# Kernel optimization log

Measured on AMD Instinct MI355X. Metric: run time of the kernel, lower is better.

Reference implementation:

```python
import jax, jax.numpy as jnp
import numpy as np

NEG = -1.0e30  # finite stand-in for -inf (exp(NEG-x)==0 exactly in fp32, grad-safe)
PRUNE = 5


def setup_inputs() -> dict:
    key = jax.random.key(0)
    k1, k2, k3, k4 = jax.random.split(key, 4)
    B, T, U, V = 8, 192, 193, 512
    logits = jax.random.normal(k1, (B, T, U, V), dtype=jnp.float32)
    log_probs = jax.nn.log_softmax(logits, axis=-1)  # [B,T,U,V]
    targets = jax.random.randint(k2, (B, U - 1), 1, V, dtype=jnp.int32)
    # lengths must satisfy |t_len-u_len| <= PRUNE for the terminal cell to be in-band
    target_lengths = jax.random.randint(k3, (B,), 150, U, dtype=jnp.int32)
    off = jax.random.randint(k4, (B,), -3, 4, dtype=jnp.int32)
    logit_lengths = jnp.clip(target_lengths + off, 1, T).astype(jnp.int32)
    return {"log_probs": log_probs, "targets": targets,
            "logit_lengths": logit_lengths, "target_lengths": target_lengths}


def _rnnt_loss(log_probs, targets, logit_lengths, target_lengths, prune_range=PRUNE):
    B, T, U, V = log_probs.shape
    Ut = targets.shape[1]  # U - 1
    dt = log_probs.dtype

    blank = log_probs[..., 0]  # [B,T,U] p_blank at (t,u)
    # emit[b,t,j] = log_probs[b,t,j,targets[b,j]]
    emit = jnp.take_along_axis(log_probs[:, :, :Ut, :], targets[:, None, :, None], axis=3)[..., 0]  # [B,T,Ut]
    # emit candidate requires t < T: pad a NEG row at t==T
    emit = jnp.concatenate([emit, jnp.full((B, 1, Ut), NEG, dt)], axis=1)  # [B,T+1,Ut]
    # g[b,t,u] = gain entering cell (t,u) from (t,u-1); g[:,:,0] unused
    g_all = jnp.concatenate([jnp.full((B, T + 1, 1), NEG, dt), emit], axis=2)  # [B,T+1,U]
    # blank_pad[:,t,:] = blank[:,t-1,:] (row t pulls blank from frame t-1); t==0 has no blank move
    blank_pad = jnp.concatenate([jnp.full((B, 1, U), NEG, dt), blank], axis=1)  # [B,T+1,U]

    u_idx = jnp.arange(U)

    def band_mask(t):
        # cells the original actually computes on row t
        return ((u_idx[None, :] >= t - prune_range)
                & (u_idx[None, :] <= t + prune_range)
                & (u_idx[None, :] <= target_lengths[:, None]))

    def combine(x, y):
        # linear recurrence r[u] = logaddexp(r[u-1] + g[u], base[u]) as an associative op
        g1, r1 = x
        g2, r2 = y
        return (g1 + g2, jnp.logaddexp(r1 + g2, r2))

    def row_from_base(base, g, t):
        base = jnp.where(band_mask(t), base, NEG)  # out-of-band cells never feed the row
        _, r = jax.lax.associative_scan(combine, (g, base), axis=1)
        return jnp.where(band_mask(t), r, NEG)

    # row 0: alpha[0,0]=0, within-row emit chain
    init_base = jnp.full((B, U), NEG, dt).at[:, 0].set(0.0)
    row0 = row_from_base(init_base, g_all[:, 0], 0)

    def step(prev, xs):
        blank_row, g_row, t = xs
        row = row_from_base(prev + blank_row, g_row, t)  # blank move from row t-1, then emit chain
        return row, row

    ts = jnp.arange(1, T + 1)
    _, rows = jax.lax.scan(step, row0,
                           (blank_pad[:, 1:].transpose(1, 0, 2),
                            g_all[:, 1:].transpose(1, 0, 2), ts))
    rows = jnp.concatenate([row0[None], rows], axis=0)  # [T+1,B,U]

    final = rows[logit_lengths, jnp.arange(B), target_lengths]  # alpha[t_len, u_len]
    return jnp.mean(-final)  # reduction='mean'


def reference(log_probs, targets, logit_lengths, target_lengths):
    return _rnnt_loss(log_probs, targets, logit_lengths, target_lengths)
```

## Files before the change

### kernel.cpp

```cpp
#include <hip/hip_runtime.h>


#define NEGV -1.0e30f
#define LOG2E 1.4426950408889634f
#define LN2   0.6931471805599453f

constexpr int Bc = 8, Tc = 192, Uc = 193, Vc = 512;
constexpr int Utc = Uc - 1;
constexpr int NCH = 16;
constexpr int CL  = 12;

#if __has_builtin(__builtin_amdgcn_exp2f)
#define EXP2(x) __builtin_amdgcn_exp2f(x)
#else
#define EXP2(x) __expf((x) * LN2)
#endif
#if __has_builtin(__builtin_amdgcn_logf)
#define LOG2(x) __builtin_amdgcn_logf(x)
#else
#define LOG2(x) (__logf(x) * LOG2E)
#endif

template <int CTRL>
__device__ __forceinline__ float dppf(float old, float x) {
    return __int_as_float(__builtin_amdgcn_update_dpp(
        __float_as_int(old), __float_as_int(x), CTRL, 0xF, 0xF, false));
}

__device__ __forceinline__ float lae2(float a, float b) {
    float m = fmaxf(a, b);
    float d = fminf(a, b) - m;
    return m + LOG2(1.0f + EXP2(d));
}

__device__ __forceinline__ float prefix_sum16(float g) {
    g += dppf<0x111>(0.0f, g);
    g += dppf<0x112>(0.0f, g);
    g += dppf<0x114>(0.0f, g);
    g += dppf<0x118>(0.0f, g);
    return g;
}

__device__ __forceinline__ float prefix_lae16(float s) {
    s = lae2(dppf<0x111>(NEGV, s), s);
    s = lae2(dppf<0x112>(NEGV, s), s);
    s = lae2(dppf<0x114>(NEGV, s), s);
    s = lae2(dppf<0x118>(NEGV, s), s);
    return s;
}

__device__ __forceinline__ float row_update(float alpha, float2 cur, int t,
                                            int tlen, int ls) {
    float base = dppf<0x101>(NEGV, alpha) + cur.x;
    float res;
    if (t == Tc) {
        res = base;
    } else {
        float G = prefix_sum16(cur.y);
        res = prefix_lae16(base - G) + G;
    }
    int u = t - 5 + ls;
    bool valid = (ls <= 10) && (u >= 0) && (u <= tlen);
    return valid ? res : NEGV;
}

__global__ void __launch_bounds__(192) rnnt_chunk_kernel(
        const float* __restrict__ lp, const int* __restrict__ targets,
        const int* __restrict__ logit_len, const int* __restrict__ target_len,
        float* __restrict__ ws) {
    __shared__ float2 rowbuf[CL * 16];

    const int b = blockIdx.x >> 4;
    const int c = blockIdx.x & 15;
    const int llen = logit_len[b];
    const int tlen = target_len[b];
    const int t0 = 1 + c * CL;

    {
        const int idx = threadIdx.x;
        const int r = idx >> 4, d = idx & 15;
        const int t = t0 + r;
        if (t <= llen) {
            const int u = t - 5 + d;
            float bl = NEGV;
            float g = 0.0f;
            if (d <= 10 && u >= 0 && u <= Uc - 1)
                bl = lp[(((size_t)b * Tc + (t - 1)) * Uc + u) * Vc] * LOG2E;
            if (d <= 10 && u >= 1 && u <= Uc - 1 && t <= Tc - 1)
                g = lp[(((size_t)b * Tc + t) * Uc + (u - 1)) * Vc
                       + targets[b * Utc + (u - 1)]] * LOG2E;
            rowbuf[idx] = make_float2(bl, g);
        }
    }
    __syncthreads();

    const int j  = threadIdx.x >> 4;
    const int ls = threadIdx.x & 15;
    if (j >= 11) return;

    float alpha = (ls == j) ? 0.0f : NEGV;
    #pragma unroll
    for (int r = 0; r < CL; ++r) {
        const int t = t0 + r;
        if (t > llen) break;
        alpha = row_update(alpha, rowbuf[r * 16 + ls], t, tlen, ls);
    }
    ws[(((size_t)(b * NCH + c) * 11 + j) << 4) + ls] = alpha;
}

__global__ void __launch_bounds__(64) rnnt_final_kernel(
        const float* __restrict__ lp, const int* __restrict__ targets,
        const int* __restrict__ logit_len, const int* __restrict__ target_len,
        const float* __restrict__ ws, float* __restrict__ out) {
    const int b = blockIdx.x;
    const int llen = logit_len[b];
    const int tlen = target_len[b];
    const int lane = threadIdx.x;
    const int ls = lane & 15;

    float g = 0.0f;
    {
        const int u = ls - 5;
        if (ls <= 10 && u >= 1)
            g = lp[((size_t)b * Tc * Uc + (u - 1)) * Vc
                   + targets[b * Utc + (u - 1)]] * LOG2E;
    }
    float v;
    {
        float G = prefix_sum16(g);
        float base = (ls == 5) ? 0.0f : NEGV;
        float res = prefix_lae16(base - G) + G;
        const int u = ls - 5;
        const bool valid = (ls <= 10) && (u >= 0) && (u <= tlen);
        v = valid ? res : NEGV;
    }

    for (int c = 0; c < NCH; ++c) {
        const size_t off = ((size_t)(b * NCH + c) * 11) << 4;
        float cand[11];
        #pragma unroll
        for (int jj = 0; jj < 11; ++jj) {
            float m = ws[off + ((size_t)jj << 4) + ls];
            float vj = __int_as_float(
                __builtin_amdgcn_readlane(__float_as_int(v), jj));
            cand[jj] = m + vj;
        }
        float a0 = lae2(cand[0], cand[1]);
        float a1 = lae2(cand[2], cand[3]);
        float a2 = lae2(cand[4], cand[5]);
        float a3 = lae2(cand[6], cand[7]);
        float a4 = lae2(cand[8], cand[9]);
        float b0 = lae2(a0, a1);
        float b1 = lae2(a2, a3);
        float b2 = lae2(a4, cand[10]);
        v = lae2(lae2(b0, b1), b2);
    }

    if (lane == tlen - llen + 5)
        atomicAdd(out, v * (-LN2 / (float)Bc));
}

extern "C" void kernel_launch(void* const* d_in, const int* in_sizes, int n_in,
                              void* d_out, int out_size, void* d_ws, size_t ws_size,
                              hipStream_t stream) {
    const float* lp    = (const float*)d_in[0];
    const int* targets = (const int*)d_in[1];
    const int* llen    = (const int*)d_in[2];
    const int* tlen    = (const int*)d_in[3];
    float* out = (float*)d_out;

    hipMemsetAsync(out, 0, sizeof(float) * out_size, stream);
    rnnt_chunk_kernel<<<Bc * NCH, 192, 0, stream>>>(
        lp, targets, llen, tlen, (float*)d_ws);
    rnnt_final_kernel<<<Bc, 64, 0, stream>>>(
        lp, targets, llen, tlen, (const float*)d_ws, out);
}
```

Baseline: 648.5 us.

## Fuse chunk and final kernels into one per-batch block with shared-memory transfer matrices

Replaces the two-kernel scheme (128 chunk blocks writing transfer matrices to a global workspace, then 8 final blocks combining them) with a single kernel that uses one 896-thread block per batch element. Each block gathers all band values for its sequence into shared memory. It then computes 5 chunk transfer matrices of 39 rows each in parallel and combines them in-block. This removes a kernel launch and the global workspace round-trip. In exchange it uses only 8 blocks on the GPU, each thread issues several serial gather loads, and the per-chunk serial recurrence is more than three times longer.

```diff
diff --git a/kernel.cpp b/kernel.cpp
--- a/kernel.cpp
+++ b/kernel.cpp
@@ -7,8 +7,10 @@
 
 constexpr int Bc = 8, Tc = 192, Uc = 193, Vc = 512;
 constexpr int Utc = Uc - 1;
-constexpr int NCH = 16;
-constexpr int CL  = 12;
+constexpr int ROWS = Tc + 1;
+constexpr int NCH = 5;
+constexpr int CL  = 39;
+constexpr int NTHR = 896;
 
 #if __has_builtin(__builtin_amdgcn_exp2f)
 #define EXP2(x) __builtin_amdgcn_exp2f(x)
@@ -64,83 +66,62 @@
     return valid ? res : NEGV;
 }
 
-__global__ void __launch_bounds__(192) rnnt_chunk_kernel(
+__global__ void __launch_bounds__(NTHR) rnnt_fused_kernel(
         const float* __restrict__ lp, const int* __restrict__ targets,
         const int* __restrict__ logit_len, const int* __restrict__ target_len,
-        float* __restrict__ ws) {
-    __shared__ float2 rowbuf[CL * 16];
+        float* __restrict__ out) {
+    __shared__ float2 rowbuf[ROWS * 16];
+    __shared__ float  mat[NCH * 11 * 16];
 
-    const int b = blockIdx.x >> 4;
-    const int c = blockIdx.x & 15;
+    const int b = blockIdx.x;
     const int llen = logit_len[b];
     const int tlen = target_len[b];
-    const int t0 = 1 + c * CL;
+    const int nrows = llen + 1;
 
-    {
-        const int idx = threadIdx.x;
-        const int r = idx >> 4, d = idx & 15;
-        const int t = t0 + r;
-        if (t <= llen) {
-            const int u = t - 5 + d;
-            float bl = NEGV;
-            float g = 0.0f;
-            if (d <= 10 && u >= 0 && u <= Uc - 1)
-                bl = lp[(((size_t)b * Tc + (t - 1)) * Uc + u) * Vc] * LOG2E;
-            if (d <= 10 && u >= 1 && u <= Uc - 1 && t <= Tc - 1)
-                g = lp[(((size_t)b * Tc + t) * Uc + (u - 1)) * Vc
-                       + targets[b * Utc + (u - 1)]] * LOG2E;
-            rowbuf[idx] = make_float2(bl, g);
-        }
+    for (int idx = threadIdx.x; idx < nrows * 16; idx += NTHR) {
+        int t = idx >> 4, d = idx & 15;
+        int u = t - 5 + d;
+        float bl = NEGV;
+        float g = 0.0f;
+        if (d <= 10 && u >= 0 && u <= Uc - 1 && t >= 1)
+            bl = lp[(((size_t)b * Tc + (t - 1)) * Uc + u) * Vc] * LOG2E;
+        if (d <= 10 && u >= 1 && u <= Uc - 1 && t <= Tc - 1)
+            g = lp[(((size_t)b * Tc + t) * Uc + (u - 1)) * Vc
+                   + targets[b * Utc + (u - 1)]] * LOG2E;
+        rowbuf[idx] = make_float2(bl, g);
     }
     __syncthreads();
 
-    const int j  = threadIdx.x >> 4;
+    const int e  = threadIdx.x >> 4;
     const int ls = threadIdx.x & 15;
-    if (j >= 11) return;
+    if (e < NCH * 11) {
+        const int c = e / 11, j = e - c * 11;
+        const int t0 = 1 + c * CL;
+        const int tend = min(t0 + CL - 1, llen);
+        float alpha = (ls == j) ? 0.0f : NEGV;
+        for (int t = t0; t <= tend; ++t)
+            alpha = row_update(alpha, rowbuf[t * 16 + ls], t, tlen, ls);
+        mat[e * 16 + ls] = alpha;
+    }
+    __syncthreads();
 
-    float alpha = (ls == j) ? 0.0f : NEGV;
-    #pragma unroll
-    for (int r = 0; r < CL; ++r) {
-        const int t = t0 + r;
-        if (t > llen) break;
-        alpha = row_update(alpha, rowbuf[r * 16 + ls], t, tlen, ls);
-    }
-    ws[(((size_t)(b * NCH + c) * 11 + j) << 4) + ls] = alpha;
-}
+    if (threadIdx.x >= 64) return;
 
-__global__ void __launch_bounds__(64) rnnt_final_kernel(
-        const float* __restrict__ lp, const int* __restrict__ targets,
-        const int* __restrict__ logit_len, const int* __restrict__ target_len,
-        const float* __restrict__ ws, float* __restrict__ out) {
-    const int b = blockIdx.x;
-    const int llen = logit_len[b];
-    const int tlen = target_len[b];
-    const int lane = threadIdx.x;
-    const int ls = lane & 15;
-
-    float g = 0.0f;
-    {
-        const int u = ls - 5;
-        if (ls <= 10 && u >= 1)
-            g = lp[((size_t)b * Tc * Uc + (u - 1)) * Vc
-                   + targets[b * Utc + (u - 1)]] * LOG2E;
-    }
     float v;
     {
-        float G = prefix_sum16(g);
+        float2 cur = rowbuf[ls];
+        float G = prefix_sum16(cur.y);
         float base = (ls == 5) ? 0.0f : NEGV;
-        float res = prefix_lae16(base - G) + G;
-        const int u = ls - 5;
-        const bool valid = (ls <= 10) && (u >= 0) && (u <= tlen);
-        v = valid ? res : NEGV;
+        float r = prefix_lae16(base - G) + G;
+        int u = ls - 5;
+        v = (ls <= 10 && u >= 0 && u <= tlen) ? r : NEGV;
     }
 
     for (int c = 0; c < NCH; ++c) {
-        const size_t off = ((size_t)(b * NCH + c) * 11) << 4;
         float cand[11];
         #pragma unroll
         for (int jj = 0; jj < 11; ++jj) {
-            float m = ws[off + ((size_t)jj << 4) + ls];
+            float m = mat[(c * 11 + jj) * 16 + ls];
             float vj = __int_as_float(
                 __builtin_amdgcn_readlane(__float_as_int(v), jj));
             cand[jj] = m + vj;
@@ -156,7 +137,7 @@
         v = lae2(lae2(b0, b1), b2);
     }
 
-    if (lane == tlen - llen + 5)
+    if ((int)threadIdx.x == tlen - llen + 5)
         atomicAdd(out, v * (-LN2 / (float)Bc));
 }
 
@@ -170,8 +151,5 @@
     float* out = (float*)d_out;
 
     hipMemsetAsync(out, 0, sizeof(float) * out_size, stream);
-    rnnt_chunk_kernel<<<Bc * NCH, 192, 0, stream>>>(
-        lp, targets, llen, tlen, (float*)d_ws);
-    rnnt_final_kernel<<<Bc, 64, 0, stream>>>(
-        lp, targets, llen, tlen, (const float*)d_ws, out);
+    rnnt_fused_kernel<<<Bc, NTHR, 0, stream>>>(lp, targets, llen, tlen, out);
 }
```

Measured after the change: 663.7 us. +2.3%, slower.
